# Performance work log

Measured on AMD Instinct MI355X. Metric: run time of the kernel, lower is better.

The kernel has to match this reference:

```python
import jax, jax.numpy as jnp
import numpy as np

B, T, IN = 4096, 512, 1
H, L = 50, 2


def setup_inputs() -> dict:
    key = jax.random.key(0)
    ks = jax.random.split(key, 11)
    s_in = 1.0 / np.sqrt(H)  # PyTorch LSTM init scale
    def u(k, shape):
        return jax.random.uniform(k, shape, jnp.float32, -s_in, s_in)
    return {
        "x": jax.random.normal(ks[0], (B, T, IN), jnp.float32),
        # layer 0 (gate order i, f, g, o stacked along first axis, like torch)
        "W_ih0": u(ks[1], (4 * H, IN)),
        "W_hh0": u(ks[2], (4 * H, H)),
        "b_ih0": u(ks[3], (4 * H,)),
        "b_hh0": u(ks[4], (4 * H,)),
        # layer 1
        "W_ih1": u(ks[5], (4 * H, H)),
        "W_hh1": u(ks[6], (4 * H, H)),
        "b_ih1": u(ks[7], (4 * H,)),
        "b_hh1": u(ks[8], (4 * H,)),
        # final linear projection hidden -> 1
        "fc_w": u(ks[9], (1, H)),
        "fc_b": u(ks[10], (1,)),
    }


def _lstm_layer(x_tbf, W_ih, W_hh, b_ih, b_hh):
    """x_tbf: [T, B, F] -> outputs [T, B, H]. Zero initial (h, c)."""
    # Precompute input contribution for all timesteps at once: [T, B, 4H]
    gates_x = jnp.einsum('tbf,gf->tbg', x_tbf, W_ih) + b_ih + b_hh

    def step(carry, gx):
        h, c = carry
        g = gx + h @ W_hh.T  # [B, 4H]
        i, f, gg, o = jnp.split(g, 4, axis=-1)
        i = jax.nn.sigmoid(i)
        f = jax.nn.sigmoid(f)
        gg = jnp.tanh(gg)
        o = jax.nn.sigmoid(o)
        c = f * c + i * gg
        h = o * jnp.tanh(c)
        return (h, c), h

    Bsz = x_tbf.shape[1]
    h0 = jnp.zeros((Bsz, W_hh.shape[1]), x_tbf.dtype)
    (_, _), hs = jax.lax.scan(step, (h0, h0), gates_x)
    return hs  # [T, B, H]


def reference(x, W_ih0, W_hh0, b_ih0, b_hh0, W_ih1, W_hh1, b_ih1, b_hh1, fc_w, fc_b):
    x_tbf = jnp.transpose(x, (1, 0, 2))  # [T, B, IN]
    h1 = _lstm_layer(x_tbf, W_ih0, W_hh0, b_ih0, b_hh0)   # [T, B, H]
    h2 = _lstm_layer(h1, W_ih1, W_hh1, b_ih1, b_hh1)      # [T, B, H]
    last = h2[-1]                                         # [B, H] == out[:, -1, :]
    return last @ fc_w.T + fc_b                           # [B, 1]
```

## Files before the change

### kernel.cpp

```cpp
#include <hip/hip_runtime.h>


typedef _Float16 half8 __attribute__((ext_vector_type(8)));
typedef float    f32x4 __attribute__((ext_vector_type(4)));

#define TT   512
#define HID  50
#define NB   16
#define LOG2E 1.44269504f

__device__ __forceinline__ float4 make_wfrag(const float* W, const float* Wx,
                                             int gate, int cell, int chunk,
                                             int quad, bool foldx, float scale) {
    half8 hv = {};
    #pragma unroll
    for (int j = 0; j < 8; ++j) {
        const int k = 32 * chunk + 8 * quad + j;
        float v = 0.0f;
        if (cell < HID) {
            if (k < HID)                 v = W[(gate * HID + cell) * HID + k] * scale;
            else if (foldx && k == HID)  v = Wx[gate * HID + cell] * scale;
        }
        hv[j] = (_Float16)v;
    }
    return __builtin_bit_cast(float4, hv);
}

__device__ __forceinline__ float cell_update(const f32x4 a, float& c) {
    const float ei = __builtin_amdgcn_exp2f(a[0]);
    const float ef = __builtin_amdgcn_exp2f(a[1]);
    const float eg = __builtin_amdgcn_exp2f(a[2]);
    const float eo = __builtin_amdgcn_exp2f(a[3]);
    const float itg = (eg - 1.0f) *
        __builtin_amdgcn_rcpf((1.0f + ei) * (eg + 1.0f));
    const float sf = __builtin_amdgcn_rcpf(1.0f + ef);
    c = sf * c + itg;
    const float ec = __builtin_amdgcn_exp2f(c * (2.0f * LOG2E));
    return (ec - 1.0f) *
        __builtin_amdgcn_rcpf((1.0f + eo) * (ec + 1.0f));
}

#define PIN(f) asm volatile("" : "+v"(f.x), "+v"(f.y), "+v"(f.z), "+v"(f.w));
#define MFMA(af, b, c) __builtin_amdgcn_mfma_f32_16x16x32_f16(__builtin_bit_cast(half8, (af)), (b), (c), 0, 0, 0)

extern "C" __global__ __launch_bounds__(832, 4)
void lstm2_mfma_kernel(const float* __restrict__ x,
                       const float* __restrict__ W_ih0, const float* __restrict__ W_hh0,
                       const float* __restrict__ b_ih0, const float* __restrict__ b_hh0,
                       const float* __restrict__ W_ih1, const float* __restrict__ W_hh1,
                       const float* __restrict__ b_ih1, const float* __restrict__ b_hh1,
                       const float* __restrict__ fc_w, const float* __restrict__ fc_b,
                       float* __restrict__ out)
{
    __shared__ _Float16 H0[2][1024];
    __shared__ _Float16 H1[2][1024];
    __shared__ float    hfin[HID * NB];

    const int tid  = threadIdx.x;
    const int lane = tid & 63;
    const int wv   = tid >> 6;
    const int b0   = blockIdx.x * NB;

    for (int i = tid; i < 1024; i += 832) {
        H0[0][i] = (_Float16)0.f; H0[1][i] = (_Float16)0.f;
        H1[0][i] = (_Float16)0.f; H1[1][i] = (_Float16)0.f;
    }

    const int quad = lane >> 4;
    const int col  = lane & 15;

    const int mrow  = lane & 15;
    const int gateA = mrow & 3;
    const int cellA = 4 * wv + (mrow >> 2);
    const float scA = (gateA == 2) ? 2.0f * LOG2E : -LOG2E;
    float4 A0c0 = make_wfrag(W_hh0, W_ih0, gateA, cellA, 0, quad, true,  scA);
    float4 A0c1 = make_wfrag(W_hh0, W_ih0, gateA, cellA, 1, quad, true,  scA);
    float4 Aic0 = make_wfrag(W_ih1, W_ih1, gateA, cellA, 0, quad, false, scA);
    float4 Aic1 = make_wfrag(W_ih1, W_ih1, gateA, cellA, 1, quad, false, scA);
    float4 Ahc0 = make_wfrag(W_hh1, W_hh1, gateA, cellA, 0, quad, false, scA);
    float4 Ahc1 = make_wfrag(W_hh1, W_hh1, gateA, cellA, 1, quad, false, scA);
    PIN(A0c0) PIN(A0c1) PIN(Aic0) PIN(Aic1) PIN(Ahc0) PIN(Ahc1)

    const int  cellD = 4 * wv + quad;
    const bool ewok  = (cellD < HID);
    f32x4 bias0, bias1;
    #pragma unroll
    for (int g = 0; g < 4; ++g) {
        const float s = (g == 2) ? 2.0f * LOG2E : -LOG2E;
        bias0[g] = ewok ? (b_ih0[g * HID + cellD] + b_hh0[g * HID + cellD]) * s : 0.f;
        bias1[g] = ewok ? (b_ih1[g * HID + cellD] + b_hh1[g * HID + cellD]) * s : 0.f;
    }
    const int wi = (cellD >> 5) * 512 + (((cellD & 31) >> 3) * 16 + col) * 8 + (cellD & 7);

    if (tid < NB) H0[0][512 + (32 + tid) * 8 + 2] = (_Float16)x[(size_t)(b0 + tid) * TT];

    float c0 = 0.f, c1 = 0.f;
    __syncthreads();

    #pragma unroll 2
    for (int u = 0; u <= TT; ++u) {
        const int pu = u & 1, pn = pu ^ 1;

        half8 b0c0 = *(half8*)(&H0[pu][lane * 8]);
        half8 b0c1 = *(half8*)(&H0[pu][512 + lane * 8]);

        float xr = 0.f;
        if (tid < NB && (u + 1) < TT)
            xr = x[(size_t)(b0 + tid) * TT + u + 1];

        if (u != TT) {
            f32x4 acc = bias0;
            acc = MFMA(A0c0, b0c0, acc);
            acc = MFMA(A0c1, b0c1, acc);
            const float h = cell_update(acc, c0);
            if (ewok) H0[pn][wi] = (_Float16)h;
        }
        if (u != 0) {
            half8 b1c0 = *(half8*)(&H1[pn][lane * 8]);
            half8 b1c1 = *(half8*)(&H1[pn][512 + lane * 8]);
            f32x4 acc = bias1;
            acc = MFMA(Aic0, b0c0, acc);
            acc = MFMA(Aic1, b0c1, acc);
            acc = MFMA(Ahc0, b1c0, acc);
            acc = MFMA(Ahc1, b1c1, acc);
            const float h = cell_update(acc, c1);
            if (ewok) {
                H1[pu][wi] = (_Float16)h;
                if (u == TT) hfin[cellD * NB + col] = h;
            }
        }
        if (tid < NB && (u + 1) < TT)
            H0[pn][512 + (32 + tid) * 8 + 2] = (_Float16)xr;
        __syncthreads();
    }

    if (tid < NB) {
        float s = fc_b[0];
        for (int k = 0; k < HID; ++k)
            s += fc_w[k] * hfin[k * NB + tid];
        out[b0 + tid] = s;
    }
}

extern "C" void kernel_launch(void* const* d_in, const int* in_sizes, int n_in,
                              void* d_out, int out_size, void* d_ws, size_t ws_size,
                              hipStream_t stream) {
    (void)in_sizes; (void)n_in; (void)d_ws; (void)ws_size; (void)out_size;
    const float* x     = (const float*)d_in[0];
    const float* W_ih0 = (const float*)d_in[1];
    const float* W_hh0 = (const float*)d_in[2];
    const float* b_ih0 = (const float*)d_in[3];
    const float* b_hh0 = (const float*)d_in[4];
    const float* W_ih1 = (const float*)d_in[5];
    const float* W_hh1 = (const float*)d_in[6];
    const float* b_ih1 = (const float*)d_in[7];
    const float* b_hh1 = (const float*)d_in[8];
    const float* fc_w  = (const float*)d_in[9];
    const float* fc_b  = (const float*)d_in[10];

    dim3 grid(4096 / NB);
    dim3 block(832);
    lstm2_mfma_kernel<<<grid, block, 0, stream>>>(
        x, W_ih0, W_hh0, b_ih0, b_hh0,
        W_ih1, W_hh1, b_ih1, b_hh1,
        fc_w, fc_b, (float*)d_out);
}
```

Baseline: 416.6 us.

## Stage x in LDS, peel first/last steps, restructure LSTM cell math

The block's whole slice of x is loaded into padded shared memory once up front, replacing a per-step global load and LDS write by 16 threads. The layer-0 input term now comes from FMAs on the accumulator seed instead of being folded into the MFMA K column. The first and last timesteps are peeled out, so the main loop has no u==0/u==TT or ewok branches and issues all LDS reads together. The cell update keeps c pre-scaled by 2·log2e and merges reciprocals into one rcp per cell. In exchange it uses about 35 KB more LDS per block, which could reduce how many blocks fit on a CU.

```diff
diff --git a/kernel.cpp b/kernel.cpp
--- a/kernel.cpp
+++ b/kernel.cpp
@@ -4,38 +4,37 @@
 typedef _Float16 half8 __attribute__((ext_vector_type(8)));
 typedef float    f32x4 __attribute__((ext_vector_type(4)));
 
-#define TT   512
-#define HID  50
-#define NB   16
+#define TT    512
+#define HID   50
+#define NB    16
+#define XST   17
 #define LOG2E 1.44269504f
 
-__device__ __forceinline__ float4 make_wfrag(const float* W, const float* Wx,
-                                             int gate, int cell, int chunk,
-                                             int quad, bool foldx, float scale) {
+__device__ __forceinline__ float4 make_wfrag(const float* W, int gate, int cell,
+                                             int chunk, int quad, float scale) {
     half8 hv = {};
     #pragma unroll
     for (int j = 0; j < 8; ++j) {
         const int k = 32 * chunk + 8 * quad + j;
         float v = 0.0f;
-        if (cell < HID) {
-            if (k < HID)                 v = W[(gate * HID + cell) * HID + k] * scale;
-            else if (foldx && k == HID)  v = Wx[gate * HID + cell] * scale;
-        }
+        if (cell < HID && k < HID) v = W[(gate * HID + cell) * HID + k] * scale;
         hv[j] = (_Float16)v;
     }
     return __builtin_bit_cast(float4, hv);
 }
 
-__device__ __forceinline__ float cell_update(const f32x4 a, float& c) {
+__device__ __forceinline__ float cell_update(const f32x4 a, float& ct) {
+    const float K  = 2.0f * LOG2E;
     const float ei = __builtin_amdgcn_exp2f(a[0]);
     const float ef = __builtin_amdgcn_exp2f(a[1]);
     const float eg = __builtin_amdgcn_exp2f(a[2]);
     const float eo = __builtin_amdgcn_exp2f(a[3]);
-    const float itg = (eg - 1.0f) *
-        __builtin_amdgcn_rcpf((1.0f + ei) * (eg + 1.0f));
-    const float sf = __builtin_amdgcn_rcpf(1.0f + ef);
-    c = sf * c + itg;
-    const float ec = __builtin_amdgcn_exp2f(c * (2.0f * LOG2E));
+    const float p  = (1.0f + ei) * (1.0f + eg);
+    const float q  = 1.0f + ef;
+    const float t1 = __builtin_fmaf(eg, K, -K);
+    const float num = __builtin_fmaf(ct, p, t1 * q);
+    ct = num * __builtin_amdgcn_rcpf(p * q);
+    const float ec = __builtin_amdgcn_exp2f(ct);
     return (ec - 1.0f) *
         __builtin_amdgcn_rcpf((1.0f + eo) * (ec + 1.0f));
 }
@@ -54,7 +53,8 @@
 {
     __shared__ _Float16 H0[2][1024];
     __shared__ _Float16 H1[2][1024];
-    __shared__ float    hfin[HID * NB];
+    __shared__ float    xs[TT * XST];
+    __shared__ float    hfin[52 * NB];
 
     const int tid  = threadIdx.x;
     const int lane = tid & 63;
@@ -65,6 +65,11 @@
         H0[0][i] = (_Float16)0.f; H0[1][i] = (_Float16)0.f;
         H1[0][i] = (_Float16)0.f; H1[1][i] = (_Float16)0.f;
     }
+    for (int i = tid; i < NB * TT; i += 832) {
+        const int row = i >> 9;
+        const int uu  = i & (TT - 1);
+        xs[uu * XST + row] = x[(size_t)(b0 + row) * TT + uu];
+    }
 
     const int quad = lane >> 4;
     const int col  = lane & 15;
@@ -73,64 +78,78 @@
     const int gateA = mrow & 3;
     const int cellA = 4 * wv + (mrow >> 2);
     const float scA = (gateA == 2) ? 2.0f * LOG2E : -LOG2E;
-    float4 A0c0 = make_wfrag(W_hh0, W_ih0, gateA, cellA, 0, quad, true,  scA);
-    float4 A0c1 = make_wfrag(W_hh0, W_ih0, gateA, cellA, 1, quad, true,  scA);
-    float4 Aic0 = make_wfrag(W_ih1, W_ih1, gateA, cellA, 0, quad, false, scA);
-    float4 Aic1 = make_wfrag(W_ih1, W_ih1, gateA, cellA, 1, quad, false, scA);
-    float4 Ahc0 = make_wfrag(W_hh1, W_hh1, gateA, cellA, 0, quad, false, scA);
-    float4 Ahc1 = make_wfrag(W_hh1, W_hh1, gateA, cellA, 1, quad, false, scA);
+    float4 A0c0 = make_wfrag(W_hh0, gateA, cellA, 0, quad, scA);
+    float4 A0c1 = make_wfrag(W_hh0, gateA, cellA, 1, quad, scA);
+    float4 Aic0 = make_wfrag(W_ih1, gateA, cellA, 0, quad, scA);
+    float4 Aic1 = make_wfrag(W_ih1, gateA, cellA, 1, quad, scA);
+    float4 Ahc0 = make_wfrag(W_hh1, gateA, cellA, 0, quad, scA);
+    float4 Ahc1 = make_wfrag(W_hh1, gateA, cellA, 1, quad, scA);
     PIN(A0c0) PIN(A0c1) PIN(Aic0) PIN(Aic1) PIN(Ahc0) PIN(Ahc1)
 
     const int  cellD = 4 * wv + quad;
     const bool ewok  = (cellD < HID);
-    f32x4 bias0, bias1;
+    f32x4 bias0, bias1, wx0;
     #pragma unroll
     for (int g = 0; g < 4; ++g) {
         const float s = (g == 2) ? 2.0f * LOG2E : -LOG2E;
         bias0[g] = ewok ? (b_ih0[g * HID + cellD] + b_hh0[g * HID + cellD]) * s : 0.f;
         bias1[g] = ewok ? (b_ih1[g * HID + cellD] + b_hh1[g * HID + cellD]) * s : 0.f;
+        wx0[g]   = ewok ? W_ih0[g * HID + cellD] * s : 0.f;
     }
     const int wi = (cellD >> 5) * 512 + (((cellD & 31) >> 3) * 16 + col) * 8 + (cellD & 7);
 
-    if (tid < NB) H0[0][512 + (32 + tid) * 8 + 2] = (_Float16)x[(size_t)(b0 + tid) * TT];
-
-    float c0 = 0.f, c1 = 0.f;
+    float ct0 = 0.f, ct1 = 0.f;
     __syncthreads();
 
+    {
+        const float xr = xs[col];
+        f32x4 acc;
+        #pragma unroll
+        for (int g = 0; g < 4; ++g) acc[g] = __builtin_fmaf(wx0[g], xr, bias0[g]);
+        const float h = cell_update(acc, ct0);
+        H0[1][wi] = (_Float16)h;
+        __syncthreads();
+    }
+
     #pragma unroll 2
-    for (int u = 0; u <= TT; ++u) {
+    for (int u = 1; u < TT; ++u) {
         const int pu = u & 1, pn = pu ^ 1;
 
-        half8 b0c0 = *(half8*)(&H0[pu][lane * 8]);
-        half8 b0c1 = *(half8*)(&H0[pu][512 + lane * 8]);
+        const half8 b0c0 = *(const half8*)(&H0[pu][lane * 8]);
+        const half8 b0c1 = *(const half8*)(&H0[pu][512 + lane * 8]);
+        const half8 b1c0 = *(const half8*)(&H1[pn][lane * 8]);
+        const half8 b1c1 = *(const half8*)(&H1[pn][512 + lane * 8]);
+        const float xr   = xs[u * XST + col];
 
-        float xr = 0.f;
-        if (tid < NB && (u + 1) < TT)
-            xr = x[(size_t)(b0 + tid) * TT + u + 1];
+        f32x4 t;
+        #pragma unroll
+        for (int g = 0; g < 4; ++g) t[g] = __builtin_fmaf(wx0[g], xr, bias0[g]);
+        f32x4 acc0 = MFMA(A0c0, b0c0, t);
+        acc0 = MFMA(A0c1, b0c1, acc0);
 
-        if (u != TT) {
-            f32x4 acc = bias0;
-            acc = MFMA(A0c0, b0c0, acc);
-            acc = MFMA(A0c1, b0c1, acc);
-            const float h = cell_update(acc, c0);
-            if (ewok) H0[pn][wi] = (_Float16)h;
-        }
-        if (u != 0) {
-            half8 b1c0 = *(half8*)(&H1[pn][lane * 8]);
-            half8 b1c1 = *(half8*)(&H1[pn][512 + lane * 8]);
-            f32x4 acc = bias1;
-            acc = MFMA(Aic0, b0c0, acc);
-            acc = MFMA(Aic1, b0c1, acc);
-            acc = MFMA(Ahc0, b1c0, acc);
-            acc = MFMA(Ahc1, b1c1, acc);
-            const float h = cell_update(acc, c1);
-            if (ewok) {
-                H1[pu][wi] = (_Float16)h;
-                if (u == TT) hfin[cellD * NB + col] = h;
-            }
-        }
-        if (tid < NB && (u + 1) < TT)
-            H0[pn][512 + (32 + tid) * 8 + 2] = (_Float16)xr;
+        f32x4 acc1 = MFMA(Aic0, b0c0, bias1);
+        acc1 = MFMA(Aic1, b0c1, acc1);
+        acc1 = MFMA(Ahc0, b1c0, acc1);
+        acc1 = MFMA(Ahc1, b1c1, acc1);
+
+        const float h0n = cell_update(acc0, ct0);
+        H0[pn][wi] = (_Float16)h0n;
+        const float h1n = cell_update(acc1, ct1);
+        H1[pu][wi] = (_Float16)h1n;
+        __syncthreads();
+    }
+
+    {
+        const half8 b0c0 = *(const half8*)(&H0[0][lane * 8]);
+        const half8 b0c1 = *(const half8*)(&H0[0][512 + lane * 8]);
+        const half8 b1c0 = *(const half8*)(&H1[1][lane * 8]);
+        const half8 b1c1 = *(const half8*)(&H1[1][512 + lane * 8]);
+        f32x4 acc1 = MFMA(Aic0, b0c0, bias1);
+        acc1 = MFMA(Aic1, b0c1, acc1);
+        acc1 = MFMA(Ahc0, b1c0, acc1);
+        acc1 = MFMA(Ahc1, b1c1, acc1);
+        const float h1n = cell_update(acc1, ct1);
+        hfin[cellD * NB + col] = h1n;
         __syncthreads();
     }
 
```

Result: faster. 386.9 us (-7.1%).
